# Performance work log

Hardware: AMD Instinct MI355X
Metric: run time of the kernel (lower is better)

The kernel has to match this reference:

```python
import jax, jax.numpy as jnp
import numpy as np

K = 7          # kernel_size (window)
PAD = (K - 1) // 2  # SAME padding for stride 1


def setup_inputs() -> dict:
    key = jax.random.key(0)
    ks = jax.random.split(key, 7)
    B, H, W, C, F = 8, 128, 128, 256, 256
    rs = F // 2  # rel_size
    return {
        "x": jax.random.normal(ks[0], (B, H, W, C), jnp.float32),
        "Wq": jax.random.normal(ks[1], (C, F), jnp.float32) * 0.05,
        "Wk": jax.random.normal(ks[2], (C, F), jnp.float32) * 0.05,
        "Wv": jax.random.normal(ks[3], (C, F), jnp.float32) * 0.05,
        "rel_x": jax.random.normal(ks[4], (rs, K), jnp.float32) * 0.05,
        "rel_y": jax.random.normal(ks[5], (F - rs, K), jnp.float32) * 0.05,
        "bias": jax.random.normal(ks[6], (1, 1, 1, F), jnp.float32) * (1.0 / np.sqrt(F).astype(np.float32)),
    }


def reference(x, Wq, Wk, Wv, rel_x, rel_y, bias):
    B, H, W, C = x.shape
    rs = rel_x.shape[0]
    # 1x1 conv projections (single group)
    q = jnp.einsum('bhwc,cf->bhwf', x, Wq)
    k = jnp.einsum('bhwc,cf->bhwf', x, Wk)
    v = jnp.einsum('bhwc,cf->bhwf', x, Wv)
    kp = jnp.pad(k, ((0, 0), (PAD, PAD), (PAD, PAD), (0, 0)))
    vp = jnp.pad(v, ((0, 0), (PAD, PAD), (PAD, PAD), (0, 0)))
    # window scores: sum_c q * shifted(k) -> [b,h,w,kh,kw]; avoids im2col blowup
    scores = jnp.stack([
        jnp.stack([jnp.einsum('bhwf,bhwf->bhw', q, kp[:, i:i + H, j:j + W, :])
                   for j in range(K)], axis=-1)
        for i in range(K)], axis=-2)
    # relative position terms: x-half broadcasts along rows (kh), y-half along cols (kw)
    qx = jnp.einsum('bhwx,xk->bhwk', q[..., :rs], rel_x)
    qy = jnp.einsum('bhwy,yk->bhwk', q[..., rs:], rel_y)
    scores = scores + qx[:, :, :, None, :] + qy[:, :, :, :, None]
    attn = jax.nn.softmax(scores.reshape(B, H, W, K * K), axis=-1).reshape(B, H, W, K, K)
    # attention-weighted sum over the window for each channel
    out = sum(attn[:, :, :, i, j][..., None] * vp[:, i:i + H, j:j + W, :]
              for i in range(K) for j in range(K))
    return out + bias
```

## Files before the change

kernel.cpp:

```cpp
#include <hip/hip_runtime.h>
#include <hip/hip_fp16.h>
#include <stdint.h>

typedef _Float16 half8 __attribute__((ext_vector_type(8)));
typedef _Float16 half2v __attribute__((ext_vector_type(2)));
typedef __attribute__((ext_vector_type(4))) float f32x4;

__device__ __forceinline__ unsigned short f2h(float f) {
  __half h = __float2half(f);
  unsigned short u; __builtin_memcpy(&u, &h, 2); return u;
}
__device__ __forceinline__ unsigned pk2h(float a, float b) {
  auto v = __builtin_amdgcn_cvt_pkrtz(a, b);
  unsigned u; __builtin_memcpy(&u, &v, 4); return u;
}
__device__ __forceinline__ half2v h2cast(unsigned u) {
  half2v v; __builtin_memcpy(&v, &u, 4); return v;
}

#if __has_builtin(__builtin_amdgcn_fdot2)
__device__ __forceinline__ float dot2(half2v a, half2v b, float c) {
  return __builtin_amdgcn_fdot2(a, b, c, false);
}
#else
__device__ __forceinline__ float dot2(half2v a, half2v b, float c) {
  return c + (float)a[0] * (float)b[0] + (float)a[1] * (float)b[1];
}
#endif

__device__ __forceinline__ void gl_lds16(const void* g, void* l) {
  __builtin_amdgcn_global_load_lds(
      (const __attribute__((address_space(1))) void*)g,
      (__attribute__((address_space(3))) void*)l, 16, 0, 0);
}

__global__ __launch_bounds__(256) void xcvt(const float* __restrict__ x,
                                            unsigned short* __restrict__ xh) {
  const size_t i = ((size_t)blockIdx.x * 256 + threadIdx.x) * 8;
  float4 a = *(const float4*)&x[i];
  float4 b = *(const float4*)&x[i + 4];
  uint4 o;
  o.x = pk2h(a.x, a.y); o.y = pk2h(a.z, a.w);
  o.z = pk2h(b.x, b.y); o.w = pk2h(b.z, b.w);
  *(uint4*)&xh[i] = o;
}

__global__ __launch_bounds__(256) void wconv(const float* __restrict__ Wq,
                                             const float* __restrict__ Wk,
                                             const float* __restrict__ Wv,
                                             unsigned short* __restrict__ Wb) {
  const int e = blockIdx.x;
  const int w = e >> 8;
  const int n = e & 255;
  const float* W = (w == 0) ? Wq : ((w == 1) ? Wk : Wv);
  const int k = threadIdx.x;
  Wb[(size_t)e * 256 + k] = f2h(W[(size_t)k * 256 + n]);
}

__global__ __launch_bounds__(256) void qkv_gemm(const unsigned short* __restrict__ xh,
                                                const unsigned short* __restrict__ Wb,
                                                unsigned short* __restrict__ qkv) {
  __shared__ unsigned char ldsb[32768];

  const int tid = threadIdx.x;
  const int l = tid & 63, l15 = l & 15, l4 = l >> 4;
  const int wv = tid >> 6, wr = wv >> 1, wc = wv & 1;

  const int pid = blockIdx.x;
  const int cid = (pid & 7) * 768 + (pid >> 3);
  const int by = cid / 6;
  const int bx = cid - by * 6;
  const size_t row0 = (size_t)by * 128;
  const int n0 = bx * 128;

  const int rbase0 = wv * 32, rbase1 = wv * 32 + 16;
  const int rA0 = rbase0 + (l >> 2), rA1 = rbase1 + (l >> 2);
  const int q0 = (l & 3) ^ ((rA0 >> 1) & 3), q1 = (l & 3) ^ ((rA1 >> 1) & 3);
  const unsigned short* gA0 = xh + (row0 + rA0) * 256 + q0 * 8;
  const unsigned short* gA1 = xh + (row0 + rA1) * 256 + q1 * 8;
  const unsigned short* gB0 = Wb + (size_t)(n0 + rA0) * 256 + q0 * 8;
  const unsigned short* gB1 = Wb + (size_t)(n0 + rA1) * 256 + q1 * 8;

  f32x4 acc[4][4] = {};

  auto stage = [&](int s, int d) {
    gl_lds16(gA0 + s * 32, &ldsb[d * 8192 + rbase0 * 64]);
    gl_lds16(gA1 + s * 32, &ldsb[d * 8192 + rbase1 * 64]);
    gl_lds16(gB0 + s * 32, &ldsb[16384 + d * 8192 + rbase0 * 64]);
    gl_lds16(gB1 + s * 32, &ldsb[16384 + d * 8192 + rbase1 * 64]);
  };

  stage(0, 0);
  __syncthreads();

  for (int s = 0; s < 8; ++s) {
    const int d = s & 1;
    if (s < 7) stage(s + 1, d ^ 1);
    half8 af[4], bf[4];
#pragma unroll
    for (int m = 0; m < 4; ++m) {
      const int r = wr * 64 + m * 16 + l15;
      af[m] = *(const half8*)&ldsb[d * 8192 + r * 64 + ((l4 ^ ((r >> 1) & 3)) * 16)];
    }
#pragma unroll
    for (int n = 0; n < 4; ++n) {
      const int r = wc * 64 + n * 16 + l15;
      bf[n] = *(const half8*)&ldsb[16384 + d * 8192 + r * 64 + ((l4 ^ ((r >> 1) & 3)) * 16)];
    }
#pragma unroll
    for (int n = 0; n < 4; ++n)
#pragma unroll
      for (int m = 0; m < 4; ++m)
        acc[m][n] = __builtin_amdgcn_mfma_f32_16x16x32_f16(af[m], bf[n], acc[m][n], 0, 0, 0);
    __syncthreads();
  }

#pragma unroll
  for (int m = 0; m < 4; ++m)
#pragma unroll
    for (int n = 0; n < 4; ++n) {
      const int ng = n0 + wc * 64 + n * 16 + l15;
      unsigned short* op = qkv + (size_t)(ng >> 8) * 33554432 + (ng & 255);
#pragma unroll
      for (int r = 0; r < 4; ++r) {
        const size_t grow = row0 + wr * 64 + m * 16 + l4 * 4 + r;
        op[grow * 256] = f2h(acc[m][n][r]);
      }
    }
}

__global__ __launch_bounds__(256) void qrel(const unsigned short* __restrict__ q,
                                            const float* __restrict__ relx,
                                            const float* __restrict__ rely,
                                            unsigned short* __restrict__ qr) {
  __shared__ unsigned wpk[896];
  for (int i = threadIdx.x; i < 896; i += 256) {
    const int hf = (i >= 448) ? 1 : 0;
    const int r = i - hf * 448;
    const int c2 = r / 7, j = r - c2 * 7;
    const float* R = hf ? rely : relx;
    wpk[i] = pk2h(R[(2 * c2) * 7 + j], R[(2 * c2 + 1) * 7 + j]);
  }
  __syncthreads();
  const size_t pix = (size_t)blockIdx.x * 256 + threadIdx.x;
  const uint4* qp = (const uint4*)(q + pix * 256);
  float ax[7] = {0, 0, 0, 0, 0, 0, 0}, ay[7] = {0, 0, 0, 0, 0, 0, 0};
#pragma unroll
  for (int g = 0; g < 32; ++g) {
    const uint4 u = qp[g];
    const int c2b = (g & 15) * 4;
    if (g < 16) {
#pragma unroll
      for (int j = 0; j < 7; ++j) {
        float s = ax[j];
        s = dot2(h2cast(u.x), h2cast(wpk[(c2b + 0) * 7 + j]), s);
        s = dot2(h2cast(u.y), h2cast(wpk[(c2b + 1) * 7 + j]), s);
        s = dot2(h2cast(u.z), h2cast(wpk[(c2b + 2) * 7 + j]), s);
        s = dot2(h2cast(u.w), h2cast(wpk[(c2b + 3) * 7 + j]), s);
        ax[j] = s;
      }
    } else {
#pragma unroll
      for (int j = 0; j < 7; ++j) {
        float s = ay[j];
        s = dot2(h2cast(u.x), h2cast(wpk[448 + (c2b + 0) * 7 + j]), s);
        s = dot2(h2cast(u.y), h2cast(wpk[448 + (c2b + 1) * 7 + j]), s);
        s = dot2(h2cast(u.z), h2cast(wpk[448 + (c2b + 2) * 7 + j]), s);
        s = dot2(h2cast(u.w), h2cast(wpk[448 + (c2b + 3) * 7 + j]), s);
        ay[j] = s;
      }
    }
  }
  uint4 o0, o1;
  o0.x = pk2h(ax[0], ax[1]); o0.y = pk2h(ax[2], ax[3]);
  o0.z = pk2h(ax[4], ax[5]); o0.w = pk2h(ax[6], ay[0]);
  o1.x = pk2h(ay[1], ay[2]); o1.y = pk2h(ay[3], ay[4]);
  o1.z = pk2h(ay[5], ay[6]); o1.w = 0;
  uint4* dst = (uint4*)(qr + pix * 512);
  dst[0] = o0; dst[1] = o1;
}

__global__ __launch_bounds__(256) void attn(const unsigned short* __restrict__ qkv,
                                            const float* __restrict__ bias,
                                            const unsigned short* __restrict__ qrelb,
                                            float* __restrict__ out) {
  __shared__ unsigned short kv[2][4][4256];

  const int tid = threadIdx.x;
  const int col = tid & 31, row = tid >> 5;

  const int pid = blockIdx.x;
  const int cid = (pid & 7) * 64 + (pid >> 3);
  const int ht = cid & 15, wt = (cid >> 4) & 3, b = cid >> 6;

  const int h = ht * 8 + row, w = wt * 32 + col;
  const size_t pix = (size_t)((b * 128 + h) * 128 + w);
  const int pbase = row * 38 + col;

  const unsigned short* qb = qkv;
  const unsigned short* kb = qkv + 33554432;
  const unsigned short* vb = qkv + 67108864;

  const int pr0 = tid / 38, pc0 = tid - pr0 * 38;
  const int gh0 = ht * 8 + pr0 - 3, gw0 = wt * 32 + pc0 - 3;
  const bool ok0 = ((unsigned)gh0 < 128u) && ((unsigned)gw0 < 128u);
  const long long go0 = ((long long)((b * 128 + gh0) * 128 + gw0)) * 256;

  const int p1 = tid + 256;
  const int pr1 = p1 / 38, pc1 = p1 - pr1 * 38;
  const int gh1 = ht * 8 + pr1 - 3, gw1 = wt * 32 + pc1 - 3;
  const bool ok1 = ((unsigned)gh1 < 128u) && ((unsigned)gw1 < 128u);
  const long long go1 = ((long long)((b * 128 + gh1) * 128 + gw1)) * 256;

  const int p2 = tid + 512;
  const int pr2 = p2 / 38, pc2 = p2 - pr2 * 38;
  const int gh2 = ht * 8 + pr2 - 3, gw2 = wt * 32 + pc2 - 3;
  const bool ok2 = (p2 < 532) && ((unsigned)gh2 < 128u) && ((unsigned)gw2 < 128u);
  const long long go2 = ((long long)((b * 128 + gh2) * 128 + gw2)) * 256;

  const int wb8 = (tid >> 6) * 512;

  auto stage = [&](const unsigned short* base, int c, int d) {
#pragma unroll
    for (int g = 0; g < 4; ++g) {
      if (ok0) gl_lds16(base + go0 + c * 32 + g * 8, &kv[d][g][wb8]);
      if (ok1) gl_lds16(base + go1 + c * 32 + g * 8, &kv[d][g][2048 + wb8]);
      if (ok2) gl_lds16(base + go2 + c * 32 + g * 8, &kv[d][g][4096]);
    }
  };

  {
    const uint4 z = make_uint4(0u, 0u, 0u, 0u);
    for (int p = tid; p < 532; p += 256) {
      const int pr = p / 38, pc = p - pr * 38;
      const int gh = ht * 8 + pr - 3, gw = wt * 32 + pc - 3;
      if (!((unsigned)gh < 128u && (unsigned)gw < 128u)) {
#pragma unroll
        for (int d = 0; d < 2; ++d)
#pragma unroll
          for (int g = 0; g < 4; ++g)
            *(uint4*)&kv[d][g][p * 8] = z;
      }
    }
  }

  float qx[7], qy[7];
  {
    const uint4* rp = (const uint4*)(qrelb + pix * 512);
    uint4 r0 = rp[0], r1 = rp[1];
    half2v a0 = h2cast(r0.x), a1 = h2cast(r0.y), a2 = h2cast(r0.z), a3 = h2cast(r0.w);
    half2v b0 = h2cast(r1.x), b1 = h2cast(r1.y), b2 = h2cast(r1.z);
    qx[0] = a0[0]; qx[1] = a0[1]; qx[2] = a1[0]; qx[3] = a1[1];
    qx[4] = a2[0]; qx[5] = a2[1]; qx[6] = a3[0];
    qy[0] = a3[1]; qy[1] = b0[0]; qy[2] = b0[1]; qy[3] = b1[0];
    qy[4] = b1[1]; qy[5] = b2[0]; qy[6] = b2[1];
  }

  stage(kb, 0, 0);
  __syncthreads();

  float sc[49];
#pragma unroll
  for (int t = 0; t < 49; ++t) sc[t] = 0.0f;

  for (int s = 0; s < 8; ++s) {
    const int d = s & 1;
    stage(s < 7 ? kb : vb, s < 7 ? s + 1 : 0, d ^ 1);
    const uint4* qsrc = (const uint4*)(qb + pix * 256 + s * 32);
    uint4 u0 = qsrc[0], u1 = qsrc[1], u2 = qsrc[2], u3 = qsrc[3];
    half2v qh[16];
    qh[0] = h2cast(u0.x); qh[1] = h2cast(u0.y); qh[2] = h2cast(u0.z); qh[3] = h2cast(u0.w);
    qh[4] = h2cast(u1.x); qh[5] = h2cast(u1.y); qh[6] = h2cast(u1.z); qh[7] = h2cast(u1.w);
    qh[8] = h2cast(u2.x); qh[9] = h2cast(u2.y); qh[10] = h2cast(u2.z); qh[11] = h2cast(u2.w);
    qh[12] = h2cast(u3.x); qh[13] = h2cast(u3.y); qh[14] = h2cast(u3.z); qh[15] = h2cast(u3.w);
    __builtin_amdgcn_s_setprio(1);
#pragma unroll
    for (int i = 0; i < 7; ++i)
#pragma unroll
      for (int j = 0; j < 7; ++j) {
        const int q8 = (pbase + i * 38 + j) * 8;
        uint4 k0 = *(const uint4*)&kv[d][0][q8];
        uint4 k1 = *(const uint4*)&kv[d][1][q8];
        uint4 k2 = *(const uint4*)&kv[d][2][q8];
        uint4 k3 = *(const uint4*)&kv[d][3][q8];
        float s2 = sc[i * 7 + j];
        s2 = dot2(h2cast(k0.x), qh[0], s2);  s2 = dot2(h2cast(k0.y), qh[1], s2);
        s2 = dot2(h2cast(k0.z), qh[2], s2);  s2 = dot2(h2cast(k0.w), qh[3], s2);
        s2 = dot2(h2cast(k1.x), qh[4], s2);  s2 = dot2(h2cast(k1.y), qh[5], s2);
        s2 = dot2(h2cast(k1.z), qh[6], s2);  s2 = dot2(h2cast(k1.w), qh[7], s2);
        s2 = dot2(h2cast(k2.x), qh[8], s2);  s2 = dot2(h2cast(k2.y), qh[9], s2);
        s2 = dot2(h2cast(k2.z), qh[10], s2); s2 = dot2(h2cast(k2.w), qh[11], s2);
        s2 = dot2(h2cast(k3.x), qh[12], s2); s2 = dot2(h2cast(k3.y), qh[13], s2);
        s2 = dot2(h2cast(k3.z), qh[14], s2); s2 = dot2(h2cast(k3.w), qh[15], s2);
        sc[i * 7 + j] = s2;
      }
    __builtin_amdgcn_s_setprio(0);
    __syncthreads();
  }

#pragma unroll
  for (int i = 0; i < 7; ++i)
#pragma unroll
    for (int j = 0; j < 7; ++j) sc[i * 7 + j] += qx[j] + qy[i];
  float mx = sc[0];
#pragma unroll
  for (int t = 1; t < 49; ++t) mx = fmaxf(mx, sc[t]);
  float sum = 0.0f;
#pragma unroll
  for (int t = 0; t < 49; ++t) {
    float e = __expf(sc[t] - mx);
    sc[t] = e;
    sum += e;
  }
  const float invs = 1.0f / sum;
  unsigned pw[49];
#pragma unroll
  for (int t = 0; t < 49; ++t) {
    const unsigned short ph = f2h(sc[t] * invs);
    pw[t] = (unsigned)ph | ((unsigned)ph << 16);
  }

  for (int s = 0; s < 8; ++s) {
    const int d = s & 1;
    const int f0 = s * 32;
    if (s < 7) stage(vb, s + 1, d ^ 1);
    half2v acc[16];
#pragma unroll
    for (int a = 0; a < 16; ++a) acc[a] = half2v{(_Float16)0, (_Float16)0};
    __builtin_amdgcn_s_setprio(1);
#pragma unroll
    for (int i = 0; i < 7; ++i)
#pragma unroll
      for (int j = 0; j < 7; ++j) {
        const int q8 = (pbase + i * 38 + j) * 8;
        uint4 v0 = *(const uint4*)&kv[d][0][q8];
        uint4 v1 = *(const uint4*)&kv[d][1][q8];
        uint4 v2 = *(const uint4*)&kv[d][2][q8];
        uint4 v3 = *(const uint4*)&kv[d][3][q8];
        const half2v p2h = h2cast(pw[i * 7 + j]);
        acc[0] += p2h * h2cast(v0.x);  acc[1] += p2h * h2cast(v0.y);
        acc[2] += p2h * h2cast(v0.z);  acc[3] += p2h * h2cast(v0.w);
        acc[4] += p2h * h2cast(v1.x);  acc[5] += p2h * h2cast(v1.y);
        acc[6] += p2h * h2cast(v1.z);  acc[7] += p2h * h2cast(v1.w);
        acc[8] += p2h * h2cast(v2.x);  acc[9] += p2h * h2cast(v2.y);
        acc[10] += p2h * h2cast(v2.z); acc[11] += p2h * h2cast(v2.w);
        acc[12] += p2h * h2cast(v3.x); acc[13] += p2h * h2cast(v3.y);
        acc[14] += p2h * h2cast(v3.z); acc[15] += p2h * h2cast(v3.w);
      }
    __builtin_amdgcn_s_setprio(0);
#pragma unroll
    for (int fq = 0; fq < 8; ++fq) {
      float4 bv = *(const float4*)&bias[f0 + fq * 4];
      float4 o;
      o.x = (float)acc[fq * 2 + 0][0] + bv.x;
      o.y = (float)acc[fq * 2 + 0][1] + bv.y;
      o.z = (float)acc[fq * 2 + 1][0] + bv.z;
      o.w = (float)acc[fq * 2 + 1][1] + bv.w;
      *(float4*)&out[pix * 256 + f0 + fq * 4] = o;
    }
    if (s < 7) __syncthreads();
  }
}

extern "C" void kernel_launch(void* const* d_in, const int* in_sizes, int n_in,
                              void* d_out, int out_size, void* d_ws, size_t ws_size,
                              hipStream_t stream) {
  const float* x = (const float*)d_in[0];
  const float* Wq = (const float*)d_in[1];
  const float* Wk = (const float*)d_in[2];
  const float* Wv = (const float*)d_in[3];
  const float* relx = (const float*)d_in[4];
  const float* rely = (const float*)d_in[5];
  const float* bias = (const float*)d_in[6];
  float* out = (float*)d_out;

  unsigned short* xh = (unsigned short*)d_out;
  unsigned short* qrl = (unsigned short*)d_out;
  unsigned short* Wb = (unsigned short*)d_ws;
  unsigned short* qkv = (unsigned short*)((char*)d_ws + 393216);

  xcvt<<<dim3(16384), dim3(256), 0, stream>>>(x, xh);
  wconv<<<dim3(768), dim3(256), 0, stream>>>(Wq, Wk, Wv, Wb);
  qkv_gemm<<<dim3(6144), dim3(256), 0, stream>>>(xh, Wb, qkv);
  qrel<<<dim3(512), dim3(256), 0, stream>>>(qkv, relx, rely, qrl);
  attn<<<dim3(512), dim3(256), 0, stream>>>(qkv, bias, qrl, out);
}
```

Baseline: 281.2 us.

## Compute two vertically adjacent pixels per thread to reuse window K/V loads

The attention kernel now has each thread handle two pixels in adjacent rows, with the tile growing from 8x32 to 16x32 output pixels and the halo to 22x38. Each LDS row of K/V loaded for one window row is shared by both pixels' score and weighted-sum accumulation, which cuts LDS reads per output roughly in half and amortizes halo staging. In exchange, register pressure doubles (two 49-entry score arrays, two accumulator sets) and LDS use rises. The grid halves to 256 blocks, which can leave CUs underused and lower occupancy.

```diff
diff --git a/kernel.cpp b/kernel.cpp
--- a/kernel.cpp
+++ b/kernel.cpp
@@ -184,56 +184,53 @@
                                             const float* __restrict__ bias,
                                             const unsigned short* __restrict__ qrelb,
                                             float* __restrict__ out) {
-  __shared__ unsigned short kv[2][4][4256];
+  __shared__ unsigned short kv[2][4][6688];
 
   const int tid = threadIdx.x;
-  const int col = tid & 31, row = tid >> 5;
+  const int tc = tid & 31, tr = tid >> 5;
 
   const int pid = blockIdx.x;
-  const int cid = (pid & 7) * 64 + (pid >> 3);
-  const int ht = cid & 15, wt = (cid >> 4) & 3, b = cid >> 6;
-
-  const int h = ht * 8 + row, w = wt * 32 + col;
-  const size_t pix = (size_t)((b * 128 + h) * 128 + w);
-  const int pbase = row * 38 + col;
+  const int cid = (pid & 7) * 32 + (pid >> 3);
+  const int b = cid >> 5;
+  const int t5 = cid & 31;
+  const int ht = t5 >> 2, wt = t5 & 3;
+
+  const int rA = ht * 16 + 2 * tr;
+  const int w = wt * 32 + tc;
+  const size_t pixA = (size_t)((b * 128 + rA) * 128 + w);
+  const size_t pixB = pixA + 128;
 
   const unsigned short* qb = qkv;
   const unsigned short* kb = qkv + 33554432;
   const unsigned short* vb = qkv + 67108864;
 
-  const int pr0 = tid / 38, pc0 = tid - pr0 * 38;
-  const int gh0 = ht * 8 + pr0 - 3, gw0 = wt * 32 + pc0 - 3;
-  const bool ok0 = ((unsigned)gh0 < 128u) && ((unsigned)gw0 < 128u);
-  const long long go0 = ((long long)((b * 128 + gh0) * 128 + gw0)) * 256;
-
-  const int p1 = tid + 256;
-  const int pr1 = p1 / 38, pc1 = p1 - pr1 * 38;
-  const int gh1 = ht * 8 + pr1 - 3, gw1 = wt * 32 + pc1 - 3;
-  const bool ok1 = ((unsigned)gh1 < 128u) && ((unsigned)gw1 < 128u);
-  const long long go1 = ((long long)((b * 128 + gh1) * 128 + gw1)) * 256;
-
-  const int p2 = tid + 512;
-  const int pr2 = p2 / 38, pc2 = p2 - pr2 * 38;
-  const int gh2 = ht * 8 + pr2 - 3, gw2 = wt * 32 + pc2 - 3;
-  const bool ok2 = (p2 < 532) && ((unsigned)gh2 < 128u) && ((unsigned)gw2 < 128u);
-  const long long go2 = ((long long)((b * 128 + gh2) * 128 + gw2)) * 256;
-
+  long long go[4];
+  bool ok[4];
+#pragma unroll
+  for (int k = 0; k < 4; ++k) {
+    const int p = tid + k * 256;
+    const int pr = p / 38, pc = p - pr * 38;
+    const int gh = ht * 16 + pr - 3, gw = wt * 32 + pc - 3;
+    ok[k] = (p < 836) && ((unsigned)gh < 128u) && ((unsigned)gw < 128u);
+    go[k] = ((long long)((b * 128 + gh) * 128 + gw)) * 256;
+  }
   const int wb8 = (tid >> 6) * 512;
 
   auto stage = [&](const unsigned short* base, int c, int d) {
 #pragma unroll
     for (int g = 0; g < 4; ++g) {
-      if (ok0) gl_lds16(base + go0 + c * 32 + g * 8, &kv[d][g][wb8]);
-      if (ok1) gl_lds16(base + go1 + c * 32 + g * 8, &kv[d][g][2048 + wb8]);
-      if (ok2) gl_lds16(base + go2 + c * 32 + g * 8, &kv[d][g][4096]);
+#pragma unroll
+      for (int k = 0; k < 4; ++k) {
+        if (ok[k]) gl_lds16(base + go[k] + c * 32 + g * 8, &kv[d][g][k * 2048 + wb8]);
+      }
     }
   };
 
   {
     const uint4 z = make_uint4(0u, 0u, 0u, 0u);
-    for (int p = tid; p < 532; p += 256) {
+    for (int p = tid; p < 836; p += 256) {
       const int pr = p / 38, pc = p - pr * 38;
-      const int gh = ht * 8 + pr - 3, gw = wt * 32 + pc - 3;
+      const int gh = ht * 16 + pr - 3, gw = wt * 32 + pc - 3;
       if (!((unsigned)gh < 128u && (unsigned)gw < 128u)) {
 #pragma unroll
         for (int d = 0; d < 2; ++d)
@@ -244,119 +241,160 @@
     }
   }
 
-  float qx[7], qy[7];
-  {
-    const uint4* rp = (const uint4*)(qrelb + pix * 512);
-    uint4 r0 = rp[0], r1 = rp[1];
-    half2v a0 = h2cast(r0.x), a1 = h2cast(r0.y), a2 = h2cast(r0.z), a3 = h2cast(r0.w);
-    half2v b0 = h2cast(r1.x), b1 = h2cast(r1.y), b2 = h2cast(r1.z);
-    qx[0] = a0[0]; qx[1] = a0[1]; qx[2] = a1[0]; qx[3] = a1[1];
-    qx[4] = a2[0]; qx[5] = a2[1]; qx[6] = a3[0];
-    qy[0] = a3[1]; qy[1] = b0[0]; qy[2] = b0[1]; qy[3] = b1[0];
-    qy[4] = b1[1]; qy[5] = b2[0]; qy[6] = b2[1];
-  }
-
   stage(kb, 0, 0);
   __syncthreads();
 
-  float sc[49];
-#pragma unroll
-  for (int t = 0; t < 49; ++t) sc[t] = 0.0f;
+  float scA[49], scB[49];
+#pragma unroll
+  for (int t = 0; t < 49; ++t) { scA[t] = 0.0f; scB[t] = 0.0f; }
 
   for (int s = 0; s < 8; ++s) {
     const int d = s & 1;
     stage(s < 7 ? kb : vb, s < 7 ? s + 1 : 0, d ^ 1);
-    const uint4* qsrc = (const uint4*)(qb + pix * 256 + s * 32);
-    uint4 u0 = qsrc[0], u1 = qsrc[1], u2 = qsrc[2], u3 = qsrc[3];
-    half2v qh[16];
-    qh[0] = h2cast(u0.x); qh[1] = h2cast(u0.y); qh[2] = h2cast(u0.z); qh[3] = h2cast(u0.w);
-    qh[4] = h2cast(u1.x); qh[5] = h2cast(u1.y); qh[6] = h2cast(u1.z); qh[7] = h2cast(u1.w);
-    qh[8] = h2cast(u2.x); qh[9] = h2cast(u2.y); qh[10] = h2cast(u2.z); qh[11] = h2cast(u2.w);
-    qh[12] = h2cast(u3.x); qh[13] = h2cast(u3.y); qh[14] = h2cast(u3.z); qh[15] = h2cast(u3.w);
+    const uint4* qAp = (const uint4*)(qb + pixA * 256 + s * 32);
+    const uint4* qBp = (const uint4*)(qb + pixB * 256 + s * 32);
+    uint4 a0 = qAp[0], a1 = qAp[1], a2 = qAp[2], a3 = qAp[3];
+    uint4 b0 = qBp[0], b1 = qBp[1], b2 = qBp[2], b3 = qBp[3];
+    half2v qhA[16], qhB[16];
+    qhA[0] = h2cast(a0.x); qhA[1] = h2cast(a0.y); qhA[2] = h2cast(a0.z); qhA[3] = h2cast(a0.w);
+    qhA[4] = h2cast(a1.x); qhA[5] = h2cast(a1.y); qhA[6] = h2cast(a1.z); qhA[7] = h2cast(a1.w);
+    qhA[8] = h2cast(a2.x); qhA[9] = h2cast(a2.y); qhA[10] = h2cast(a2.z); qhA[11] = h2cast(a2.w);
+    qhA[12] = h2cast(a3.x); qhA[13] = h2cast(a3.y); qhA[14] = h2cast(a3.z); qhA[15] = h2cast(a3.w);
+    qhB[0] = h2cast(b0.x); qhB[1] = h2cast(b0.y); qhB[2] = h2cast(b0.z); qhB[3] = h2cast(b0.w);
+    qhB[4] = h2cast(b1.x); qhB[5] = h2cast(b1.y); qhB[6] = h2cast(b1.z); qhB[7] = h2cast(b1.w);
+    qhB[8] = h2cast(b2.x); qhB[9] = h2cast(b2.y); qhB[10] = h2cast(b2.z); qhB[11] = h2cast(b2.w);
+    qhB[12] = h2cast(b3.x); qhB[13] = h2cast(b3.y); qhB[14] = h2cast(b3.z); qhB[15] = h2cast(b3.w);
     __builtin_amdgcn_s_setprio(1);
 #pragma unroll
-    for (int i = 0; i < 7; ++i)
-#pragma unroll
-      for (int j = 0; j < 7; ++j) {
-        const int q8 = (pbase + i * 38 + j) * 8;
-        uint4 k0 = *(const uint4*)&kv[d][0][q8];
-        uint4 k1 = *(const uint4*)&kv[d][1][q8];
-        uint4 k2 = *(const uint4*)&kv[d][2][q8];
-        uint4 k3 = *(const uint4*)&kv[d][3][q8];
-        float s2 = sc[i * 7 + j];
-        s2 = dot2(h2cast(k0.x), qh[0], s2);  s2 = dot2(h2cast(k0.y), qh[1], s2);
-        s2 = dot2(h2cast(k0.z), qh[2], s2);  s2 = dot2(h2cast(k0.w), qh[3], s2);
-        s2 = dot2(h2cast(k1.x), qh[4], s2);  s2 = dot2(h2cast(k1.y), qh[5], s2);
-        s2 = dot2(h2cast(k1.z), qh[6], s2);  s2 = dot2(h2cast(k1.w), qh[7], s2);
-        s2 = dot2(h2cast(k2.x), qh[8], s2);  s2 = dot2(h2cast(k2.y), qh[9], s2);
-        s2 = dot2(h2cast(k2.z), qh[10], s2); s2 = dot2(h2cast(k2.w), qh[11], s2);
-        s2 = dot2(h2cast(k3.x), qh[12], s2); s2 = dot2(h2cast(k3.y), qh[13], s2);
-        s2 = dot2(h2cast(k3.z), qh[14], s2); s2 = dot2(h2cast(k3.w), qh[15], s2);
-        sc[i * 7 + j] = s2;
-      }
+    for (int u = 0; u < 8; ++u) {
+#pragma unroll
+      for (int g = 0; g < 4; ++g) {
+        uint4 kk[7];
+#pragma unroll
+        for (int j = 0; j < 7; ++j)
+          kk[j] = *(const uint4*)&kv[d][g][((2 * tr + u) * 38 + tc + j) * 8];
+#pragma unroll
+        for (int j = 0; j < 7; ++j) {
+          if (u < 7) {
+            float s2 = scA[u * 7 + j];
+            s2 = dot2(h2cast(kk[j].x), qhA[g * 4 + 0], s2);
+            s2 = dot2(h2cast(kk[j].y), qhA[g * 4 + 1], s2);
+            s2 = dot2(h2cast(kk[j].z), qhA[g * 4 + 2], s2);
+            s2 = dot2(h2cast(kk[j].w), qhA[g * 4 + 3], s2);
+            scA[u * 7 + j] = s2;
+          }
+          if (u >= 1) {
+            float s2 = scB[(u - 1) * 7 + j];
+            s2 = dot2(h2cast(kk[j].x), qhB[g * 4 + 0], s2);
+            s2 = dot2(h2cast(kk[j].y), qhB[g * 4 + 1], s2);
+            s2 = dot2(h2cast(kk[j].z), qhB[g * 4 + 2], s2);
+            s2 = dot2(h2cast(kk[j].w), qhB[g * 4 + 3], s2);
+            scB[(u - 1) * 7 + j] = s2;
+          }
+        }
+      }
+    }
     __builtin_amdgcn_s_setprio(0);
     __syncthreads();
   }
 
-#pragma unroll
-  for (int i = 0; i < 7; ++i)
-#pragma unroll
-    for (int j = 0; j < 7; ++j) sc[i * 7 + j] += qx[j] + qy[i];
-  float mx = sc[0];
-#pragma unroll
-  for (int t = 1; t < 49; ++t) mx = fmaxf(mx, sc[t]);
-  float sum = 0.0f;
-#pragma unroll
-  for (int t = 0; t < 49; ++t) {
-    float e = __expf(sc[t] - mx);
-    sc[t] = e;
-    sum += e;
-  }
-  const float invs = 1.0f / sum;
-  unsigned pw[49];
-#pragma unroll
-  for (int t = 0; t < 49; ++t) {
-    const unsigned short ph = f2h(sc[t] * invs);
-    pw[t] = (unsigned)ph | ((unsigned)ph << 16);
+  {
+    const uint4* rp = (const uint4*)(qrelb + pixA * 512);
+    uint4 r0 = rp[0], r1 = rp[1];
+    half2v c0 = h2cast(r0.x), c1 = h2cast(r0.y), c2 = h2cast(r0.z), c3 = h2cast(r0.w);
+    half2v c4 = h2cast(r1.x), c5 = h2cast(r1.y), c6 = h2cast(r1.z);
+    float qx[7] = {c0[0], c0[1], c1[0], c1[1], c2[0], c2[1], c3[0]};
+    float qy[7] = {c3[1], c4[0], c4[1], c5[0], c5[1], c6[0], c6[1]};
+#pragma unroll
+    for (int i = 0; i < 7; ++i)
+#pragma unroll
+      for (int j = 0; j < 7; ++j) scA[i * 7 + j] += qx[j] + qy[i];
+  }
+  {
+    const uint4* rp = (const uint4*)(qrelb + pixB * 512);
+    uint4 r0 = rp[0], r1 = rp[1];
+    half2v c0 = h2cast(r0.x), c1 = h2cast(r0.y), c2 = h2cast(r0.z), c3 = h2cast(r0.w);
+    half2v c4 = h2cast(r1.x), c5 = h2cast(r1.y), c6 = h2cast(r1.z);
+    float qx[7] = {c0[0], c0[1], c1[0], c1[1], c2[0], c2[1], c3[0]};
+    float qy[7] = {c3[1], c4[0], c4[1], c5[0], c5[1], c6[0], c6[1]};
+#pragma unroll
+    for (int i = 0; i < 7; ++i)
+#pragma unroll
+      for (int j = 0; j < 7; ++j) scB[i * 7 + j] += qx[j] + qy[i];
+  }
+
+  unsigned pwp[49];
+  {
+    float mxA = scA[0], mxB = scB[0];
+#pragma unroll
+    for (int t = 1; t < 49; ++t) { mxA = fmaxf(mxA, scA[t]); mxB = fmaxf(mxB, scB[t]); }
+    float sA = 0.0f, sB = 0.0f;
+#pragma unroll
+    for (int t = 0; t < 49; ++t) {
+      float eA = __expf(scA[t] - mxA); scA[t] = eA; sA += eA;
+      float eB = __expf(scB[t] - mxB); scB[t] = eB; sB += eB;
+    }
+    const float iA = 1.0f / sA, iB = 1.0f / sB;
+#pragma unroll
+    for (int t = 0; t < 49; ++t)
+      pwp[t] = (unsigned)f2h(scA[t] * iA) | ((unsigned)f2h(scB[t] * iB) << 16);
   }
 
   for (int s = 0; s < 8; ++s) {
     const int d = s & 1;
     const int f0 = s * 32;
     if (s < 7) stage(vb, s + 1, d ^ 1);
-    half2v acc[16];
-#pragma unroll
-    for (int a = 0; a < 16; ++a) acc[a] = half2v{(_Float16)0, (_Float16)0};
+    half2v accA[16], accB[16];
+#pragma unroll
+    for (int a = 0; a < 16; ++a) {
+      accA[a] = half2v{(_Float16)0, (_Float16)0};
+      accB[a] = half2v{(_Float16)0, (_Float16)0};
+    }
     __builtin_amdgcn_s_setprio(1);
 #pragma unroll
-    for (int i = 0; i < 7; ++i)
-#pragma unroll
-      for (int j = 0; j < 7; ++j) {
-        const int q8 = (pbase + i * 38 + j) * 8;
-        uint4 v0 = *(const uint4*)&kv[d][0][q8];
-        uint4 v1 = *(const uint4*)&kv[d][1][q8];
-        uint4 v2 = *(const uint4*)&kv[d][2][q8];
-        uint4 v3 = *(const uint4*)&kv[d][3][q8];
-        const half2v p2h = h2cast(pw[i * 7 + j]);
-        acc[0] += p2h * h2cast(v0.x);  acc[1] += p2h * h2cast(v0.y);
-        acc[2] += p2h * h2cast(v0.z);  acc[3] += p2h * h2cast(v0.w);
-        acc[4] += p2h * h2cast(v1.x);  acc[5] += p2h * h2cast(v1.y);
-        acc[6] += p2h * h2cast(v1.z);  acc[7] += p2h * h2cast(v1.w);
-        acc[8] += p2h * h2cast(v2.x);  acc[9] += p2h * h2cast(v2.y);
-        acc[10] += p2h * h2cast(v2.z); acc[11] += p2h * h2cast(v2.w);
-        acc[12] += p2h * h2cast(v3.x); acc[13] += p2h * h2cast(v3.y);
-        acc[14] += p2h * h2cast(v3.z); acc[15] += p2h * h2cast(v3.w);
-      }
+    for (int u = 0; u < 8; ++u) {
+#pragma unroll
+      for (int g = 0; g < 4; ++g) {
+        uint4 kk[7];
+#pragma unroll
+        for (int j = 0; j < 7; ++j)
+          kk[j] = *(const uint4*)&kv[d][g][((2 * tr + u) * 38 + tc + j) * 8];
+#pragma unroll
+        for (int j = 0; j < 7; ++j) {
+          if (u < 7) {
+            unsigned pa = pwp[u * 7 + j] & 0xffffu; pa |= pa << 16;
+            const half2v p2 = h2cast(pa);
+            accA[g * 4 + 0] += p2 * h2cast(kk[j].x);
+            accA[g * 4 + 1] += p2 * h2cast(kk[j].y);
+            accA[g * 4 + 2] += p2 * h2cast(kk[j].z);
+            accA[g * 4 + 3] += p2 * h2cast(kk[j].w);
+          }
+          if (u >= 1) {
+            unsigned pbv = pwp[(u - 1) * 7 + j] >> 16; pbv |= pbv << 16;
+            const half2v p2 = h2cast(pbv);
+            accB[g * 4 + 0] += p2 * h2cast(kk[j].x);
+            accB[g * 4 + 1] += p2 * h2cast(kk[j].y);
+            accB[g * 4 + 2] += p2 * h2cast(kk[j].z);
+            accB[g * 4 + 3] += p2 * h2cast(kk[j].w);
+          }
+        }
+      }
+    }
     __builtin_amdgcn_s_setprio(0);
 #pragma unroll
     for (int fq = 0; fq < 8; ++fq) {
       float4 bv = *(const float4*)&bias[f0 + fq * 4];
-      float4 o;
-      o.x = (float)acc[fq * 2 + 0][0] + bv.x;
-      o.y = (float)acc[fq * 2 + 0][1] + bv.y;
-      o.z = (float)acc[fq * 2 + 1][0] + bv.z;
-      o.w = (float)acc[fq * 2 + 1][1] + bv.w;
-      *(float4*)&out[pix * 256 + f0 + fq * 4] = o;
+      float4 oA, oB;
+      oA.x = (float)accA[fq * 2 + 0][0] + bv.x;
+      oA.y = (float)accA[fq * 2 + 0][1] + bv.y;
+      oA.z = (float)accA[fq * 2 + 1][0] + bv.z;
+      oA.w = (float)accA[fq * 2 + 1][1] + bv.w;
+      oB.x = (float)accB[fq * 2 + 0][0] + bv.x;
+      oB.y = (float)accB[fq * 2 + 0][1] + bv.y;
+      oB.z = (float)accB[fq * 2 + 1][0] + bv.z;
+      oB.w = (float)accB[fq * 2 + 1][1] + bv.w;
+      *(float4*)&out[pixA * 256 + f0 + fq * 4] = oA;
+      *(float4*)&out[pixB * 256 + f0 + fq * 4] = oB;
     }
     if (s < 7) __syncthreads();
   }
@@ -383,5 +421,5 @@
   wconv<<<dim3(768), dim3(256), 0, stream>>>(Wq, Wk, Wv, Wb);
   qkv_gemm<<<dim3(6144), dim3(256), 0, stream>>>(xh, Wb, qkv);
   qrel<<<dim3(512), dim3(256), 0, stream>>>(qkv, relx, rely, qrl);
-  attn<<<dim3(512), dim3(256), 0, stream>>>(qkv, bias, qrl, out);
-}
+  attn<<<dim3(256), dim3(256), 0, stream>>>(qkv, bias, qrl, out);
+}
```

After: 301.1 us. 7.1% more time.

## Compute window QK scores with MFMA over 2x8 query tiles and scatter via LDS

Applied to the files above, without the earlier changes.

Replaces the per-thread fdot2 score loop with 16x16x32 f16 MFMA tiles. Each wave multiplies 2x8 query pixels against a 4x14 neighborhood of keys, then scatters only the valid 7x7 window entries into an LDS score buffer that each thread reads back. This moves the QK dot products onto matrix cores, at the cost of redundant computation for out-of-window pairs, extra LDS traffic and extra barriers. The V stage is no longer prefetched during the last K step; it is staged only after the LDS buffer is reused.

```diff
diff --git a/kernel.cpp b/kernel.cpp
--- a/kernel.cpp
+++ b/kernel.cpp
@@ -188,6 +188,8 @@
 
   const int tid = threadIdx.x;
   const int col = tid & 31, row = tid >> 5;
+  const int wv = tid >> 6;
+  const int l = tid & 63, lo = l & 15, hi = l >> 4;
 
   const int pid = blockIdx.x;
   const int cid = (pid & 7) * 64 + (pid >> 3);
@@ -218,7 +220,7 @@
   const bool ok2 = (p2 < 532) && ((unsigned)gh2 < 128u) && ((unsigned)gw2 < 128u);
   const long long go2 = ((long long)((b * 128 + gh2) * 128 + gw2)) * 256;
 
-  const int wb8 = (tid >> 6) * 512;
+  const int wb8 = wv * 512;
 
   auto stage = [&](const unsigned short* base, int c, int d) {
 #pragma unroll
@@ -229,7 +231,7 @@
     }
   };
 
-  {
+  auto zero_oob = [&]() {
     const uint4 z = make_uint4(0u, 0u, 0u, 0u);
     for (int p = tid; p < 532; p += 256) {
       const int pr = p / 38, pc = p - pr * 38;
@@ -242,7 +244,81 @@
             *(uint4*)&kv[d][g][p * 8] = z;
       }
     }
-  }
+  };
+
+  zero_oob();
+  stage(kb, 0, 0);
+  __syncthreads();
+
+  int slot0[7];
+#pragma unroll
+  for (int t = 0; t < 7; ++t) {
+    const int p = t * 16 + lo;
+    const int ur = p / 14, uc = p - ur * 14;
+    slot0[t] = (2 * wv + ur) * 38 + uc;
+  }
+  const size_t qpix = (size_t)((b * 128 + ht * 8 + 2 * wv + (lo >> 3)) * 128 + wt * 32 + (lo & 7));
+  const unsigned short* qlane = qb + qpix * 256 + hi * 8;
+
+  f32x4 acc[4][7] = {};
+
+  for (int s = 0; s < 8; ++s) {
+    const int d = s & 1;
+    if (s < 7) stage(kb, s + 1, d ^ 1);
+    half8 qf[4];
+#pragma unroll
+    for (int g = 0; g < 4; ++g)
+      qf[g] = *(const half8*)(qlane + (size_t)g * 2048 + s * 32);
+    const unsigned short* kpl = &kv[d][hi][0];
+    __builtin_amdgcn_s_setprio(1);
+#pragma unroll
+    for (int t = 0; t < 7; ++t) {
+      const unsigned short* kt = kpl + slot0[t] * 8;
+#pragma unroll
+      for (int g = 0; g < 4; ++g) {
+        const half8 kf = *(const half8*)(kt + g * 64);
+        acc[g][t] = __builtin_amdgcn_mfma_f32_16x16x32_f16(qf[g], kf, acc[g][t], 0, 0, 0);
+      }
+    }
+    __builtin_amdgcn_s_setprio(0);
+    __syncthreads();
+  }
+
+  float* pbuf = (float*)&kv[0][0][0];
+#pragma unroll
+  for (int t = 0; t < 7; ++t) {
+    const int p = t * 16 + lo;
+    const int ur = p / 14, uc = p - ur * 14;
+#pragma unroll
+    for (int r = 0; r < 4; ++r) {
+      const int qq = hi * 4 + r;
+      const int di = ur - (qq >> 3), dj = uc - (qq & 7);
+      if (((unsigned)di < 7u) && ((unsigned)dj < 7u)) {
+        const int prow_ = wv * 64 + (qq >> 3) * 32 + (qq & 7);
+        const int pslot = di * 7 + dj;
+#pragma unroll
+        for (int g = 0; g < 4; ++g)
+          pbuf[(prow_ + g * 8) * 52 + pslot] = acc[g][t][r];
+      }
+    }
+  }
+  __syncthreads();
+
+  float sc[49];
+  {
+    const float* prow = pbuf + tid * 52;
+#pragma unroll
+    for (int k = 0; k < 12; ++k) {
+      const float4 v = ((const float4*)prow)[k];
+      sc[k * 4 + 0] = v.x; sc[k * 4 + 1] = v.y;
+      sc[k * 4 + 2] = v.z; sc[k * 4 + 3] = v.w;
+    }
+    sc[48] = prow[48];
+  }
+  __syncthreads();
+
+  zero_oob();
+  stage(vb, 0, 0);
 
   float qx[7], qy[7];
   {
@@ -256,48 +332,6 @@
     qy[4] = b1[1]; qy[5] = b2[0]; qy[6] = b2[1];
   }
 
-  stage(kb, 0, 0);
-  __syncthreads();
-
-  float sc[49];
-#pragma unroll
-  for (int t = 0; t < 49; ++t) sc[t] = 0.0f;
-
-  for (int s = 0; s < 8; ++s) {
-    const int d = s & 1;
-    stage(s < 7 ? kb : vb, s < 7 ? s + 1 : 0, d ^ 1);
-    const uint4* qsrc = (const uint4*)(qb + pix * 256 + s * 32);
-    uint4 u0 = qsrc[0], u1 = qsrc[1], u2 = qsrc[2], u3 = qsrc[3];
-    half2v qh[16];
-    qh[0] = h2cast(u0.x); qh[1] = h2cast(u0.y); qh[2] = h2cast(u0.z); qh[3] = h2cast(u0.w);
-    qh[4] = h2cast(u1.x); qh[5] = h2cast(u1.y); qh[6] = h2cast(u1.z); qh[7] = h2cast(u1.w);
-    qh[8] = h2cast(u2.x); qh[9] = h2cast(u2.y); qh[10] = h2cast(u2.z); qh[11] = h2cast(u2.w);
-    qh[12] = h2cast(u3.x); qh[13] = h2cast(u3.y); qh[14] = h2cast(u3.z); qh[15] = h2cast(u3.w);
-    __builtin_amdgcn_s_setprio(1);
-#pragma unroll
-    for (int i = 0; i < 7; ++i)
-#pragma unroll
-      for (int j = 0; j < 7; ++j) {
-        const int q8 = (pbase + i * 38 + j) * 8;
-        uint4 k0 = *(const uint4*)&kv[d][0][q8];
-        uint4 k1 = *(const uint4*)&kv[d][1][q8];
-        uint4 k2 = *(const uint4*)&kv[d][2][q8];
-        uint4 k3 = *(const uint4*)&kv[d][3][q8];
-        float s2 = sc[i * 7 + j];
-        s2 = dot2(h2cast(k0.x), qh[0], s2);  s2 = dot2(h2cast(k0.y), qh[1], s2);
-        s2 = dot2(h2cast(k0.z), qh[2], s2);  s2 = dot2(h2cast(k0.w), qh[3], s2);
-        s2 = dot2(h2cast(k1.x), qh[4], s2);  s2 = dot2(h2cast(k1.y), qh[5], s2);
-        s2 = dot2(h2cast(k1.z), qh[6], s2);  s2 = dot2(h2cast(k1.w), qh[7], s2);
-        s2 = dot2(h2cast(k2.x), qh[8], s2);  s2 = dot2(h2cast(k2.y), qh[9], s2);
-        s2 = dot2(h2cast(k2.z), qh[10], s2); s2 = dot2(h2cast(k2.w), qh[11], s2);
-        s2 = dot2(h2cast(k3.x), qh[12], s2); s2 = dot2(h2cast(k3.y), qh[13], s2);
-        s2 = dot2(h2cast(k3.z), qh[14], s2); s2 = dot2(h2cast(k3.w), qh[15], s2);
-        sc[i * 7 + j] = s2;
-      }
-    __builtin_amdgcn_s_setprio(0);
-    __syncthreads();
-  }
-
 #pragma unroll
   for (int i = 0; i < 7; ++i)
 #pragma unroll
@@ -319,14 +353,15 @@
     const unsigned short ph = f2h(sc[t] * invs);
     pw[t] = (unsigned)ph | ((unsigned)ph << 16);
   }
+  __syncthreads();
 
   for (int s = 0; s < 8; ++s) {
     const int d = s & 1;
     const int f0 = s * 32;
     if (s < 7) stage(vb, s + 1, d ^ 1);
-    half2v acc[16];
-#pragma unroll
-    for (int a = 0; a < 16; ++a) acc[a] = half2v{(_Float16)0, (_Float16)0};
+    half2v acc2[16];
+#pragma unroll
+    for (int a = 0; a < 16; ++a) acc2[a] = half2v{(_Float16)0, (_Float16)0};
     __builtin_amdgcn_s_setprio(1);
 #pragma unroll
     for (int i = 0; i < 7; ++i)
@@ -338,24 +373,24 @@
         uint4 v2 = *(const uint4*)&kv[d][2][q8];
         uint4 v3 = *(const uint4*)&kv[d][3][q8];
         const half2v p2h = h2cast(pw[i * 7 + j]);
-        acc[0] += p2h * h2cast(v0.x);  acc[1] += p2h * h2cast(v0.y);
-        acc[2] += p2h * h2cast(v0.z);  acc[3] += p2h * h2cast(v0.w);
-        acc[4] += p2h * h2cast(v1.x);  acc[5] += p2h * h2cast(v1.y);
-        acc[6] += p2h * h2cast(v1.z);  acc[7] += p2h * h2cast(v1.w);
-        acc[8] += p2h * h2cast(v2.x);  acc[9] += p2h * h2cast(v2.y);
-        acc[10] += p2h * h2cast(v2.z); acc[11] += p2h * h2cast(v2.w);
-        acc[12] += p2h * h2cast(v3.x); acc[13] += p2h * h2cast(v3.y);
-        acc[14] += p2h * h2cast(v3.z); acc[15] += p2h * h2cast(v3.w);
+        acc2[0] += p2h * h2cast(v0.x);  acc2[1] += p2h * h2cast(v0.y);
+        acc2[2] += p2h * h2cast(v0.z);  acc2[3] += p2h * h2cast(v0.w);
+        acc2[4] += p2h * h2cast(v1.x);  acc2[5] += p2h * h2cast(v1.y);
+        acc2[6] += p2h * h2cast(v1.z);  acc2[7] += p2h * h2cast(v1.w);
+        acc2[8] += p2h * h2cast(v2.x);  acc2[9] += p2h * h2cast(v2.y);
+        acc2[10] += p2h * h2cast(v2.z); acc2[11] += p2h * h2cast(v2.w);
+        acc2[12] += p2h * h2cast(v3.x); acc2[13] += p2h * h2cast(v3.y);
+        acc2[14] += p2h * h2cast(v3.z); acc2[15] += p2h * h2cast(v3.w);
       }
     __builtin_amdgcn_s_setprio(0);
 #pragma unroll
     for (int fq = 0; fq < 8; ++fq) {
       float4 bv = *(const float4*)&bias[f0 + fq * 4];
       float4 o;
-      o.x = (float)acc[fq * 2 + 0][0] + bv.x;
-      o.y = (float)acc[fq * 2 + 0][1] + bv.y;
-      o.z = (float)acc[fq * 2 + 1][0] + bv.z;
-      o.w = (float)acc[fq * 2 + 1][1] + bv.w;
+      o.x = (float)acc2[fq * 2 + 0][0] + bv.x;
+      o.y = (float)acc2[fq * 2 + 0][1] + bv.y;
+      o.z = (float)acc2[fq * 2 + 1][0] + bv.z;
+      o.w = (float)acc2[fq * 2 + 1][1] + bv.w;
       *(float4*)&out[pix * 256 + f0 + fq * 4] = o;
     }
     if (s < 7) __syncthreads();
```

Result: slower. 300.4 us (+6.8%).
